# Kernel optimization log

Measured on AMD Instinct MI355X. Metric: run time of the kernel, lower is better.

The kernel has to match this reference:

```python
import jax, jax.numpy as jnp
import numpy as np

EPS = 1e-12  # torch F.normalize default eps


def setup_inputs() -> dict:
    key = jax.random.key(0)
    k1, k2, k3, k4 = jax.random.split(key, 4)
    N, M, V, F, H = 8192, 8192, 3, 512, 512
    common_z = jax.random.normal(k1, (N, F), dtype=jnp.float32)
    zs = jax.random.normal(k2, (V, M, F), dtype=jnp.float32)
    # torch nn.Linear weights have shape [out, in]; kaiming-uniform-ish scale
    s = 1.0 / np.sqrt(F)
    Wq = jax.random.uniform(k3, (H, F), dtype=jnp.float32, minval=-s, maxval=s)
    Wk = jax.random.uniform(k4, (H, F), dtype=jnp.float32, minval=-s, maxval=s)
    return {"common_z": common_z, "zs": zs, "Wq": Wq, "Wk": Wk, "view_num": V}


def reference(common_z, zs, Wq, Wk, view_num):
    # q: [N, H]
    q = jax.nn.elu(common_z @ Wq.T)
    out = common_z
    # view_num is a small fixed structural constant (3); loop over views,
    # matching the original per-view accumulation into common_z.
    for v in range(view_num):
        zv = zs[v]                          # [M, F]
        k = jax.nn.elu(zv @ Wk.T)           # [M, H]
        att = q @ k.T                       # [N, M]
        # row-wise L2 normalize (torch F.normalize p=2, dim=-1)
        norm = jnp.sqrt(jnp.sum(att * att, axis=-1, keepdims=True))
        att = att / jnp.maximum(norm, EPS)
        out = out + att @ zv                # [N, F]
    return out
```

## Files before the change

### kernel.cpp

```cpp
#include <hip/hip_runtime.h>
#include <cstdint>

#define NROWS 8192
#define MDIM  8192
#define FDIM  512
#define HDIM  512
#define GWSPLIT 4

typedef _Float16 f16x8_t __attribute__((ext_vector_type(8)));
typedef float    f32x4_t __attribute__((ext_vector_type(4)));
typedef int      i32x4_t __attribute__((ext_vector_type(4)));

__device__ __forceinline__ unsigned short f2h(float f) {
    return __builtin_bit_cast(unsigned short, (_Float16)f);
}
__device__ __forceinline__ float h2f(unsigned short u) {
    return (float)__builtin_bit_cast(_Float16, u);
}

__device__ __forceinline__ void g2l16(const unsigned short* g, unsigned short* l) {
    __builtin_amdgcn_global_load_lds(
        (const __attribute__((address_space(1))) void*)g,
        (__attribute__((address_space(3))) void*)l, 16, 0, 0);
}

__global__ void k_prep(const float* __restrict__ zs,
                       unsigned short* __restrict__ zn,
                       unsigned short* __restrict__ zt, long tV,
                       const float* __restrict__ cz, unsigned short* __restrict__ cz_h,
                       const float* __restrict__ Wq, unsigned short* __restrict__ wq_h,
                       const float* __restrict__ Wk, unsigned short* __restrict__ wk_h) {
    const long MF = (long)MDIM * FDIM;
    int z = blockIdx.z;
    if (z < 3) {
        const float* src = zs + (long)z * MF;
        unsigned short* dn = zn + (long)z * MF;
        unsigned short* dt = zt + (long)z * tV;
        __shared__ unsigned short t[32][33];
        int c0 = blockIdx.x * 32, r0 = blockIdx.y * 32;
        #pragma unroll
        for (int k = 0; k < 32; k += 8) {
            unsigned short b = f2h(src[(size_t)(r0 + threadIdx.y + k) * FDIM + c0 + threadIdx.x]);
            dn[(size_t)(r0 + threadIdx.y + k) * FDIM + c0 + threadIdx.x] = b;
            t[threadIdx.y + k][threadIdx.x] = b;
        }
        __syncthreads();
        #pragma unroll
        for (int k = 0; k < 32; k += 8)
            dt[(size_t)(c0 + threadIdx.y + k) * MDIM + r0 + threadIdx.x] =
                t[threadIdx.x][threadIdx.y + k];
    } else {
        int tid = threadIdx.y * 32 + threadIdx.x;
        int b = blockIdx.y * gridDim.x + blockIdx.x;
        if (z == 3) {
            int i = b * 256 + tid;
            float4 f = ((const float4*)cz)[i];
            ushort4 u;
            u.x = f2h(f.x); u.y = f2h(f.y); u.z = f2h(f.z); u.w = f2h(f.w);
            ((ushort4*)cz_h)[i] = u;
        } else if (b < 512) {
            const float4* s = (b < 256) ? (const float4*)Wq : (const float4*)Wk;
            ushort4* d = (b < 256) ? (ushort4*)wq_h : (ushort4*)wk_h;
            int i = (b & 255) * 256 + tid;
            float4 f = s[i];
            ushort4 u;
            u.x = f2h(f.x); u.y = f2h(f.y); u.z = f2h(f.z); u.w = f2h(f.w);
            d[i] = u;
        }
    }
}

__global__ void k_rsplit(const float* __restrict__ GWp,
                         unsigned short* __restrict__ G,
                         unsigned short* __restrict__ Bfin,
                         float* __restrict__ n2, int n) {
    int i = blockIdx.x * blockDim.x + threadIdx.x;
    if (i >= n) return;
    if (i < 3 * NROWS) n2[i] = 0.f;
    int v = i / (1024 * 512);
    int rc = i - v * (1024 * 512);
    int row = rc >> 9, col = rc & 511;
    const float* p = GWp + (size_t)v * GWSPLIT * 1024 * 512 + rc;
    float s = 0.f;
    #pragma unroll
    for (int sl = 0; sl < GWSPLIT; ++sl) s += p[(size_t)sl * 1024 * 512];
    if (row < 512) G[((size_t)v * 512 + row) * 512 + col] = f2h(s);
    else Bfin[(size_t)(row - 512) * 1536 + v * 512 + col] = f2h(s);
}

template<int MODE>
__global__ __launch_bounds__(256, 2)
void k_gemm_bt(const unsigned short* __restrict__ A, int lda, long aV, int akmask,
               const unsigned short* __restrict__ B, int ldb, long bV,
               int K, int kslices,
               unsigned short* __restrict__ Cb, long cbV,
               float* __restrict__ Cf, int ldc, long cfV,
               float* __restrict__ norms,
               const unsigned short* __restrict__ Q,
               const float* __restrict__ CZ,
               const unsigned short* __restrict__ B2,
               unsigned short* __restrict__ Cb2) {
    const int z    = blockIdx.z;
    const int view = (MODE == 3) ? z / kslices : z;
    const int kbeg = (MODE == 3) ? (z % kslices) * K : 0;
    A += (long)view * aV;
    const unsigned short* Bp = (MODE == 0 && z > 0) ? B2 : B;
    Bp += (long)view * bV;

    __shared__ unsigned short S[2 * 128 * 64];
    unsigned short* As = S;
    unsigned short* Bs = S + 128 * 64;
    const int tid  = threadIdx.x;
    const int lane = tid & 63;
    const int w    = tid >> 6;
    const int wr   = w >> 1, wc = w & 1;
    const int row0 = blockIdx.y * 128;
    const int col0 = blockIdx.x * 128;
    const int quad = lane >> 4;
    const int l15  = lane & 15;
    const int srow = lane >> 3;
    const int scol = (((lane & 7) ^ srow) * 8);
    const int wbase = w * 4;

    _Float16 sch[3][4];
    if (MODE == 2) {
        #pragma unroll
        for (int v = 0; v < 3; ++v)
            #pragma unroll
            for (int i = 0; i < 4; ++i) {
                int row = row0 + wr * 64 + i * 16 + l15;
                float nn = norms[v * NROWS + row];
                float s = 1.f / fmaxf(sqrtf(fmaxf(nn, 0.f)), 1e-12f);
                sch[v][i] = (_Float16)fminf(s, 60000.f);
            }
    }

    f32x4_t acc[4][4] = {};

    for (int k0 = kbeg; k0 < kbeg + K; k0 += 64) {
        __syncthreads();
        const int ka = k0 & akmask;
        #pragma unroll
        for (int c = 0; c < 4; ++c) {
            int rr = (wbase + c) * 8 + srow;
            g2l16(A  + (size_t)(row0 + rr) * lda + ka + scol, &As[(wbase + c) * 512]);
            g2l16(Bp + (size_t)(col0 + rr) * ldb + k0 + scol, &Bs[(wbase + c) * 512]);
        }
        asm volatile("s_waitcnt vmcnt(0)" ::: "memory");
        __syncthreads();
        #pragma unroll
        for (int kk = 0; kk < 2; ++kk) {
            f16x8_t af[4], bfr[4];
            #pragma unroll
            for (int i = 0; i < 4; ++i) {
                int r = wr * 64 + i * 16 + l15;
                af[i] = __builtin_bit_cast(f16x8_t,
                        *(const i32x4_t*)&As[r * 64 + (((kk * 4 + quad) ^ (r & 7)) << 3)]);
            }
            if (MODE == 2) {
                int vw = k0 >> 9;
                #pragma unroll
                for (int i = 0; i < 4; ++i) af[i] = af[i] * sch[vw][i];
            }
            #pragma unroll
            for (int j = 0; j < 4; ++j) {
                int r = wc * 64 + j * 16 + l15;
                bfr[j] = __builtin_bit_cast(f16x8_t,
                        *(const i32x4_t*)&Bs[r * 64 + (((kk * 4 + quad) ^ (r & 7)) << 3)]);
            }
            #pragma unroll
            for (int i = 0; i < 4; ++i)
                #pragma unroll
                for (int j = 0; j < 4; ++j)
                    acc[i][j] = __builtin_amdgcn_mfma_f32_16x16x32_f16(
                        af[i], bfr[j], acc[i][j], 0, 0, 0);
        }
    }

    if (MODE == 0) {
        if (z == 0) {
            #pragma unroll
            for (int i = 0; i < 4; ++i) {
                int rb = row0 + wr * 64 + i * 16 + quad * 4;
                #pragma unroll
                for (int j = 0; j < 4; ++j) {
                    int col = col0 + wc * 64 + j * 16 + l15;
                    #pragma unroll
                    for (int r = 0; r < 4; ++r) {
                        float v = acc[i][j][r];
                        v = v > 0.f ? v : expm1f(v);
                        Cb[(size_t)(rb + r) * ldc + col] = f2h(v);
                    }
                }
            }
        } else {
            __syncthreads();
            unsigned short* T = S + w * 4096;
            #pragma unroll
            for (int i = 0; i < 4; ++i)
                #pragma unroll
                for (int j = 0; j < 4; ++j) {
                    int ct = j * 16 + l15;
                    #pragma unroll
                    for (int r = 0; r < 4; ++r) {
                        int rt = i * 16 + quad * 4 + r;
                        float v = acc[i][j][r];
                        v = v > 0.f ? v : expm1f(v);
                        T[ct * 64 + (rt ^ ((ct & 7) << 3))] = f2h(v);
                    }
                }
            unsigned short* dst = Cb2 + (long)(z - 1) * cbV;
            #pragma unroll
            for (int it = 0; it < 8; ++it) {
                int c  = it * 8 + (lane >> 3);
                int rg = (lane & 7) * 8;
                i32x4_t val = *(const i32x4_t*)&T[c * 64 + (rg ^ ((c & 7) << 3))];
                *(i32x4_t*)&dst[(size_t)(col0 + wc * 64 + c) * MDIM
                                + row0 + wr * 64 + rg] = val;
            }
        }
    } else if (MODE == 2) {
        #pragma unroll
        for (int i = 0; i < 4; ++i) {
            #pragma unroll
            for (int r = 0; r < 4; ++r) {
                int row = row0 + wr * 64 + i * 16 + quad * 4 + r;
                #pragma unroll
                for (int j = 0; j < 4; ++j) {
                    int col = col0 + wc * 64 + j * 16 + l15;
                    Cf[(size_t)row * ldc + col] =
                        CZ[(size_t)row * ldc + col] + acc[i][j][r];
                }
            }
        }
    } else if (MODE == 3) {
        float* C = Cf + (long)z * cfV;
        #pragma unroll
        for (int i = 0; i < 4; ++i) {
            int rb = row0 + wr * 64 + i * 16 + quad * 4;
            #pragma unroll
            for (int j = 0; j < 4; ++j) {
                int col = col0 + wc * 64 + j * 16 + l15;
                #pragma unroll
                for (int r = 0; r < 4; ++r)
                    C[(size_t)(rb + r) * ldc + col] = acc[i][j][r];
            }
        }
    } else if (MODE == 4) {
        float* nptr = norms + (long)view * NROWS;
        float rs[4][4] = {};
        #pragma unroll
        for (int i = 0; i < 4; ++i) {
            int rb = row0 + wr * 64 + i * 16 + quad * 4;
            #pragma unroll
            for (int j = 0; j < 4; ++j) {
                int col = col0 + wc * 64 + j * 16 + l15;
                #pragma unroll
                for (int r = 0; r < 4; ++r)
                    rs[i][r] += acc[i][j][r] * h2f(Q[(size_t)(rb + r) * ldc + col]);
            }
        }
        #pragma unroll
        for (int i = 0; i < 4; ++i)
            #pragma unroll
            for (int r = 0; r < 4; ++r) {
                float v = rs[i][r];
                v += __shfl_xor(v, 1);
                v += __shfl_xor(v, 2);
                v += __shfl_xor(v, 4);
                v += __shfl_xor(v, 8);
                if (l15 == 0)
                    atomicAdd(&nptr[row0 + wr * 64 + i * 16 + quad * 4 + r], v);
            }
    }
}

extern "C" void kernel_launch(void* const* d_in, const int* in_sizes, int n_in,
                              void* d_out, int out_size, void* d_ws, size_t ws_size,
                              hipStream_t stream) {
    const float* cz = (const float*)d_in[0];
    const float* zs = (const float*)d_in[1];
    const float* Wq = (const float*)d_in[2];
    const float* Wk = (const float*)d_in[3];
    float* out = (float*)d_out;
    const int NOMASK = 0x7fffffff;

    char* ws = (char*)d_ws;
    size_t off = 0;
    auto alloc = [&](size_t bytes) -> void* {
        void* p = ws + off;
        off += (bytes + 255) & ~(size_t)255;
        return p;
    };
    const long MF = (long)MDIM * FDIM;
    const long KZ = (long)1024 * MDIM;

    unsigned short* X_h   = (unsigned short*)alloc((size_t)4 * MF * 2);
    unsigned short* wq_h  = (unsigned short*)alloc((size_t)HDIM * FDIM * 2);
    unsigned short* wk_h  = (unsigned short*)alloc((size_t)HDIM * FDIM * 2);
    unsigned short* q_h   = (unsigned short*)alloc((size_t)NROWS * HDIM * 2);
    unsigned short* kzT   = (unsigned short*)alloc((size_t)3 * KZ * 2);
    float* GWp            = (float*)alloc((size_t)3 * GWSPLIT * 1024 * 512 * 4);
    unsigned short* G     = (unsigned short*)alloc((size_t)3 * 512 * 512 * 2);
    unsigned short* Bfin  = (unsigned short*)alloc((size_t)512 * 1536 * 2);
    float* n2             = (float*)alloc((size_t)3 * NROWS * 4);

    k_prep<<<dim3(FDIM / 32, MDIM / 32, 5), dim3(32, 8), 0, stream>>>(
        zs, X_h + MF, kzT + (size_t)512 * MDIM, KZ,
        cz, X_h, Wq, wq_h, Wk, wk_h);

    k_gemm_bt<0><<<dim3(4, 64, 4), 256, 0, stream>>>(
        X_h, FDIM, MF, NOMASK, wq_h, FDIM, 0, FDIM, 0,
        q_h, KZ, nullptr, HDIM, 0, nullptr, nullptr, nullptr, wk_h, kzT);

    k_gemm_bt<3><<<dim3(4, 8, 3 * GWSPLIT), 256, 0, stream>>>(
        kzT, MDIM, KZ, NOMASK, kzT, MDIM, KZ, MDIM / GWSPLIT, GWSPLIT,
        nullptr, 0, GWp, 512, (long)1024 * 512, nullptr, nullptr, nullptr,
        nullptr, nullptr);

    k_rsplit<<<dim3(3 * 1024 * 512 / 256), 256, 0, stream>>>(
        GWp, G, Bfin, n2, 3 * 1024 * 512);

    k_gemm_bt<4><<<dim3(4, 64, 3), 256, 0, stream>>>(
        q_h, HDIM, 0, NOMASK, G, HDIM, (long)512 * 512, HDIM, 0,
        nullptr, 0, nullptr, HDIM, 0, n2, q_h, nullptr, nullptr, nullptr);

    k_gemm_bt<2><<<dim3(4, 64, 1), 256, 0, stream>>>(
        q_h, HDIM, 0, 511, Bfin, 1536, 0, 1536, 0,
        nullptr, 0, out, FDIM, 0, n2, nullptr, cz, nullptr, nullptr);
}
```

Before: 251.8 us.

## Fuse all stages into one persistent cooperative kernel with grid syncs

Replaces the six separate kernel launches (prep, Wq/Wk projection GEMM, Gram GEMM, split reduction, norm GEMM, final GEMM) with a single cooperative persistent kernel. Each stage becomes a grid-stride job loop, and grid.sync() separates the stages. The aim is to remove launch gaps and inter-kernel idle time. The cost is that the grid size is capped at the occupancy limit, so small stages may underfill the device, and each grid barrier adds its own overhead.

```diff
diff --git a/kernel.cpp b/kernel.cpp
--- a/kernel.cpp
+++ b/kernel.cpp
@@ -1,11 +1,15 @@
 #include <hip/hip_runtime.h>
+#include <hip/hip_cooperative_groups.h>
 #include <cstdint>
+
+namespace cg = cooperative_groups;
 
 #define NROWS 8192
 #define MDIM  8192
 #define FDIM  512
 #define HDIM  512
 #define GWSPLIT 4
+#define NOMASK 0x7fffffff
 
 typedef _Float16 f16x8_t __attribute__((ext_vector_type(8)));
 typedef float    f32x4_t __attribute__((ext_vector_type(4)));
@@ -24,98 +28,42 @@
         (__attribute__((address_space(3))) void*)l, 16, 0, 0);
 }
 
-__global__ void k_prep(const float* __restrict__ zs,
-                       unsigned short* __restrict__ zn,
-                       unsigned short* __restrict__ zt, long tV,
-                       const float* __restrict__ cz, unsigned short* __restrict__ cz_h,
-                       const float* __restrict__ Wq, unsigned short* __restrict__ wq_h,
-                       const float* __restrict__ Wk, unsigned short* __restrict__ wk_h) {
-    const long MF = (long)MDIM * FDIM;
-    int z = blockIdx.z;
-    if (z < 3) {
-        const float* src = zs + (long)z * MF;
-        unsigned short* dn = zn + (long)z * MF;
-        unsigned short* dt = zt + (long)z * tV;
-        __shared__ unsigned short t[32][33];
-        int c0 = blockIdx.x * 32, r0 = blockIdx.y * 32;
-        #pragma unroll
-        for (int k = 0; k < 32; k += 8) {
-            unsigned short b = f2h(src[(size_t)(r0 + threadIdx.y + k) * FDIM + c0 + threadIdx.x]);
-            dn[(size_t)(r0 + threadIdx.y + k) * FDIM + c0 + threadIdx.x] = b;
-            t[threadIdx.y + k][threadIdx.x] = b;
-        }
-        __syncthreads();
-        #pragma unroll
-        for (int k = 0; k < 32; k += 8)
-            dt[(size_t)(c0 + threadIdx.y + k) * MDIM + r0 + threadIdx.x] =
-                t[threadIdx.x][threadIdx.y + k];
-    } else {
-        int tid = threadIdx.y * 32 + threadIdx.x;
-        int b = blockIdx.y * gridDim.x + blockIdx.x;
-        if (z == 3) {
-            int i = b * 256 + tid;
-            float4 f = ((const float4*)cz)[i];
-            ushort4 u;
-            u.x = f2h(f.x); u.y = f2h(f.y); u.z = f2h(f.z); u.w = f2h(f.w);
-            ((ushort4*)cz_h)[i] = u;
-        } else if (b < 512) {
-            const float4* s = (b < 256) ? (const float4*)Wq : (const float4*)Wk;
-            ushort4* d = (b < 256) ? (ushort4*)wq_h : (ushort4*)wk_h;
-            int i = (b & 255) * 256 + tid;
-            float4 f = s[i];
-            ushort4 u;
-            u.x = f2h(f.x); u.y = f2h(f.y); u.z = f2h(f.z); u.w = f2h(f.w);
-            d[i] = u;
-        }
-    }
-}
-
-__global__ void k_rsplit(const float* __restrict__ GWp,
-                         unsigned short* __restrict__ G,
-                         unsigned short* __restrict__ Bfin,
-                         float* __restrict__ n2, int n) {
-    int i = blockIdx.x * blockDim.x + threadIdx.x;
-    if (i >= n) return;
-    if (i < 3 * NROWS) n2[i] = 0.f;
-    int v = i / (1024 * 512);
-    int rc = i - v * (1024 * 512);
-    int row = rc >> 9, col = rc & 511;
-    const float* p = GWp + (size_t)v * GWSPLIT * 1024 * 512 + rc;
-    float s = 0.f;
-    #pragma unroll
-    for (int sl = 0; sl < GWSPLIT; ++sl) s += p[(size_t)sl * 1024 * 512];
-    if (row < 512) G[((size_t)v * 512 + row) * 512 + col] = f2h(s);
-    else Bfin[(size_t)(row - 512) * 1536 + v * 512 + col] = f2h(s);
-}
+struct MegaP {
+    const float* cz; const float* zs; const float* Wq; const float* Wk;
+    float* out;
+    unsigned short* X_h; unsigned short* wq_h; unsigned short* wk_h;
+    unsigned short* q_h; unsigned short* kzT;
+    float* GWp; unsigned short* G; unsigned short* Bfin; float* n2;
+};
 
 template<int MODE>
-__global__ __launch_bounds__(256, 2)
-void k_gemm_bt(const unsigned short* __restrict__ A, int lda, long aV, int akmask,
-               const unsigned short* __restrict__ B, int ldb, long bV,
-               int K, int kslices,
-               unsigned short* __restrict__ Cb, long cbV,
-               float* __restrict__ Cf, int ldc, long cfV,
-               float* __restrict__ norms,
-               const unsigned short* __restrict__ Q,
-               const float* __restrict__ CZ,
-               const unsigned short* __restrict__ B2,
-               unsigned short* __restrict__ Cb2) {
-    const int z    = blockIdx.z;
+__device__ __forceinline__ void gemm_tile(
+    unsigned short* S, int bx, int by, int z,
+    const unsigned short* __restrict__ A, int lda, long aV, int akmask,
+    const unsigned short* __restrict__ B, int ldb, long bV,
+    int K, int kslices,
+    unsigned short* __restrict__ Cb, long cbV, int ldc,
+    float* __restrict__ Cf, long cfV,
+    float* __restrict__ norms,
+    const unsigned short* __restrict__ Q,
+    const float* __restrict__ CZ,
+    const unsigned short* __restrict__ B2,
+    unsigned short* __restrict__ Cb2)
+{
     const int view = (MODE == 3) ? z / kslices : z;
     const int kbeg = (MODE == 3) ? (z % kslices) * K : 0;
     A += (long)view * aV;
     const unsigned short* Bp = (MODE == 0 && z > 0) ? B2 : B;
     Bp += (long)view * bV;
 
-    __shared__ unsigned short S[2 * 128 * 64];
     unsigned short* As = S;
     unsigned short* Bs = S + 128 * 64;
     const int tid  = threadIdx.x;
     const int lane = tid & 63;
     const int w    = tid >> 6;
     const int wr   = w >> 1, wc = w & 1;
-    const int row0 = blockIdx.y * 128;
-    const int col0 = blockIdx.x * 128;
+    const int row0 = by * 128;
+    const int col0 = bx * 128;
     const int quad = lane >> 4;
     const int l15  = lane & 15;
     const int srow = lane >> 3;
@@ -218,6 +166,7 @@
                 *(i32x4_t*)&dst[(size_t)(col0 + wc * 64 + c) * MDIM
                                 + row0 + wr * 64 + rg] = val;
             }
+            __syncthreads();
         }
     } else if (MODE == 2) {
         #pragma unroll
@@ -251,13 +200,14 @@
         float rs[4][4] = {};
         #pragma unroll
         for (int i = 0; i < 4; ++i) {
-            int rb = row0 + wr * 64 + i * 16 + quad * 4;
             #pragma unroll
             for (int j = 0; j < 4; ++j) {
-                int col = col0 + wc * 64 + j * 16 + l15;
-                #pragma unroll
-                for (int r = 0; r < 4; ++r)
+                #pragma unroll
+                for (int r = 0; r < 4; ++r) {
+                    int rb = row0 + wr * 64 + i * 16 + quad * 4;
+                    int col = col0 + wc * 64 + j * 16 + l15;
                     rs[i][r] += acc[i][j][r] * h2f(Q[(size_t)(rb + r) * ldc + col]);
+                }
             }
         }
         #pragma unroll
@@ -275,16 +225,109 @@
     }
 }
 
+__global__ __launch_bounds__(256, 2) void k_mega(MegaP p) {
+    __shared__ unsigned short S[2 * 128 * 64];
+    cg::grid_group grid = cg::this_grid();
+    const int nb  = gridDim.x;
+    const int tid = threadIdx.x;
+    const long MF = (long)MDIM * FDIM;
+    const long KZ = (long)1024 * MDIM;
+
+    for (int job = blockIdx.x; job < 16992; job += nb) {
+        if (job < 12288) {
+            int v = job >> 12, t = job & 4095;
+            int c0 = (t & 15) * 32, r0 = (t >> 4) * 32;
+            int lx = tid & 31, ly = tid >> 5;
+            const float* src = p.zs + (long)v * MF;
+            unsigned short* dn = p.X_h + MF + (long)v * MF;
+            unsigned short* dt = p.kzT + (size_t)512 * MDIM + (long)v * KZ;
+            unsigned short (*t33)[33] = (unsigned short(*)[33])S;
+            #pragma unroll
+            for (int k = 0; k < 32; k += 8) {
+                unsigned short b = f2h(src[(size_t)(r0 + ly + k) * FDIM + c0 + lx]);
+                dn[(size_t)(r0 + ly + k) * FDIM + c0 + lx] = b;
+                t33[ly + k][lx] = b;
+            }
+            __syncthreads();
+            #pragma unroll
+            for (int k = 0; k < 32; k += 8)
+                dt[(size_t)(c0 + ly + k) * MDIM + r0 + lx] = t33[lx][ly + k];
+            __syncthreads();
+        } else if (job < 16384) {
+            int i = (job - 12288) * 256 + tid;
+            float4 f = ((const float4*)p.cz)[i];
+            ushort4 u;
+            u.x = f2h(f.x); u.y = f2h(f.y); u.z = f2h(f.z); u.w = f2h(f.w);
+            ((ushort4*)p.X_h)[i] = u;
+        } else if (job < 16896) {
+            int b = job - 16384;
+            const float4* s = (b < 256) ? (const float4*)p.Wq : (const float4*)p.Wk;
+            ushort4* d = (b < 256) ? (ushort4*)p.wq_h : (ushort4*)p.wk_h;
+            int i = (b & 255) * 256 + tid;
+            float4 f = s[i];
+            ushort4 u;
+            u.x = f2h(f.x); u.y = f2h(f.y); u.z = f2h(f.z); u.w = f2h(f.w);
+            d[i] = u;
+        } else {
+            int idx = (job - 16896) * 256 + tid;
+            if (idx < 3 * NROWS) p.n2[idx] = 0.f;
+        }
+    }
+    grid.sync();
+
+    for (int job = blockIdx.x; job < 1024; job += nb) {
+        int z = job >> 8, r = job & 255;
+        gemm_tile<0>(S, r & 3, r >> 2, z,
+                     p.X_h, FDIM, MF, NOMASK, p.wq_h, FDIM, 0, FDIM, 0,
+                     p.q_h, KZ, HDIM, nullptr, 0,
+                     nullptr, nullptr, nullptr, p.wk_h, p.kzT);
+    }
+    grid.sync();
+
+    for (int job = blockIdx.x; job < 32 * 3 * GWSPLIT; job += nb) {
+        int z = job >> 5, r = job & 31;
+        gemm_tile<3>(S, r & 3, r >> 2, z,
+                     p.kzT, MDIM, KZ, NOMASK, p.kzT, MDIM, KZ,
+                     MDIM / GWSPLIT, GWSPLIT,
+                     nullptr, 0, 512, p.GWp, (long)1024 * 512,
+                     nullptr, nullptr, nullptr, nullptr, nullptr);
+    }
+    grid.sync();
+
+    for (int job = blockIdx.x; job < 6144; job += nb) {
+        int i = job * 256 + tid;
+        int v = i / (1024 * 512);
+        int rc = i - v * (1024 * 512);
+        int row = rc >> 9, col = rc & 511;
+        const float* q = p.GWp + (size_t)v * GWSPLIT * 1024 * 512 + rc;
+        float s = 0.f;
+        #pragma unroll
+        for (int sl = 0; sl < GWSPLIT; ++sl) s += q[(size_t)sl * 1024 * 512];
+        if (row < 512) p.G[((size_t)v * 512 + row) * 512 + col] = f2h(s);
+        else p.Bfin[(size_t)(row - 512) * 1536 + v * 512 + col] = f2h(s);
+    }
+    grid.sync();
+
+    for (int job = blockIdx.x; job < 768; job += nb) {
+        int z = job >> 8, r = job & 255;
+        gemm_tile<4>(S, r & 3, r >> 2, z,
+                     p.q_h, HDIM, 0, NOMASK, p.G, HDIM, (long)512 * 512, HDIM, 0,
+                     nullptr, 0, HDIM, nullptr, 0,
+                     p.n2, p.q_h, nullptr, nullptr, nullptr);
+    }
+    grid.sync();
+
+    for (int job = blockIdx.x; job < 256; job += nb) {
+        gemm_tile<2>(S, job & 3, job >> 2, 0,
+                     p.q_h, HDIM, 0, 511, p.Bfin, 1536, 0, 1536, 0,
+                     nullptr, 0, FDIM, p.out, 0,
+                     p.n2, nullptr, p.cz, nullptr, nullptr);
+    }
+}
+
 extern "C" void kernel_launch(void* const* d_in, const int* in_sizes, int n_in,
                               void* d_out, int out_size, void* d_ws, size_t ws_size,
                               hipStream_t stream) {
-    const float* cz = (const float*)d_in[0];
-    const float* zs = (const float*)d_in[1];
-    const float* Wq = (const float*)d_in[2];
-    const float* Wk = (const float*)d_in[3];
-    float* out = (float*)d_out;
-    const int NOMASK = 0x7fffffff;
-
     char* ws = (char*)d_ws;
     size_t off = 0;
     auto alloc = [&](size_t bytes) -> void* {
@@ -295,37 +338,29 @@
     const long MF = (long)MDIM * FDIM;
     const long KZ = (long)1024 * MDIM;
 
-    unsigned short* X_h   = (unsigned short*)alloc((size_t)4 * MF * 2);
-    unsigned short* wq_h  = (unsigned short*)alloc((size_t)HDIM * FDIM * 2);
-    unsigned short* wk_h  = (unsigned short*)alloc((size_t)HDIM * FDIM * 2);
-    unsigned short* q_h   = (unsigned short*)alloc((size_t)NROWS * HDIM * 2);
-    unsigned short* kzT   = (unsigned short*)alloc((size_t)3 * KZ * 2);
-    float* GWp            = (float*)alloc((size_t)3 * GWSPLIT * 1024 * 512 * 4);
-    unsigned short* G     = (unsigned short*)alloc((size_t)3 * 512 * 512 * 2);
-    unsigned short* Bfin  = (unsigned short*)alloc((size_t)512 * 1536 * 2);
-    float* n2             = (float*)alloc((size_t)3 * NROWS * 4);
-
-    k_prep<<<dim3(FDIM / 32, MDIM / 32, 5), dim3(32, 8), 0, stream>>>(
-        zs, X_h + MF, kzT + (size_t)512 * MDIM, KZ,
-        cz, X_h, Wq, wq_h, Wk, wk_h);
-
-    k_gemm_bt<0><<<dim3(4, 64, 4), 256, 0, stream>>>(
-        X_h, FDIM, MF, NOMASK, wq_h, FDIM, 0, FDIM, 0,
-        q_h, KZ, nullptr, HDIM, 0, nullptr, nullptr, nullptr, wk_h, kzT);
-
-    k_gemm_bt<3><<<dim3(4, 8, 3 * GWSPLIT), 256, 0, stream>>>(
-        kzT, MDIM, KZ, NOMASK, kzT, MDIM, KZ, MDIM / GWSPLIT, GWSPLIT,
-        nullptr, 0, GWp, 512, (long)1024 * 512, nullptr, nullptr, nullptr,
-        nullptr, nullptr);
-
-    k_rsplit<<<dim3(3 * 1024 * 512 / 256), 256, 0, stream>>>(
-        GWp, G, Bfin, n2, 3 * 1024 * 512);
-
-    k_gemm_bt<4><<<dim3(4, 64, 3), 256, 0, stream>>>(
-        q_h, HDIM, 0, NOMASK, G, HDIM, (long)512 * 512, HDIM, 0,
-        nullptr, 0, nullptr, HDIM, 0, n2, q_h, nullptr, nullptr, nullptr);
-
-    k_gemm_bt<2><<<dim3(4, 64, 1), 256, 0, stream>>>(
-        q_h, HDIM, 0, 511, Bfin, 1536, 0, 1536, 0,
-        nullptr, 0, out, FDIM, 0, n2, nullptr, cz, nullptr, nullptr);
-}
+    MegaP p;
+    p.cz = (const float*)d_in[0];
+    p.zs = (const float*)d_in[1];
+    p.Wq = (const float*)d_in[2];
+    p.Wk = (const float*)d_in[3];
+    p.out = (float*)d_out;
+    p.X_h  = (unsigned short*)alloc((size_t)4 * MF * 2);
+    p.wq_h = (unsigned short*)alloc((size_t)HDIM * FDIM * 2);
+    p.wk_h = (unsigned short*)alloc((size_t)HDIM * FDIM * 2);
+    p.q_h  = (unsigned short*)alloc((size_t)NROWS * HDIM * 2);
+    p.kzT  = (unsigned short*)alloc((size_t)3 * KZ * 2);
+    p.GWp  = (float*)alloc((size_t)3 * GWSPLIT * 1024 * 512 * 4);
+    p.G    = (unsigned short*)alloc((size_t)3 * 512 * 512 * 2);
+    p.Bfin = (unsigned short*)alloc((size_t)512 * 1536 * 2);
+    p.n2   = (float*)alloc((size_t)3 * NROWS * 4);
+
+    int ma = 0;
+    hipOccupancyMaxActiveBlocksPerMultiprocessor(&ma, k_mega, 256, 0);
+    if (ma < 1) ma = 1;
+    if (ma > 4) ma = 4;
+    int nblk = ma * 256;
+
+    void* args[] = {&p};
+    hipLaunchCooperativeKernel((void*)k_mega, dim3(nblk), dim3(256),
+                               args, 0, stream);
+}
```

After: 498.6 us. 98.0% more time.

## Double-buffer LDS tiles to overlap global loads with MFMA compute

Applied to the files above, without the earlier changes.

The GEMM main loop gains two LDS buffers, so the next K-tile is prefetched with global_load_lds while MFMAs run on the current one, and only the older loads are waited on (vmcnt(8)). It also raises the GW split-K factor from 4 to 8 to create more blocks. Doubling LDS to 64KB per block may limit how many blocks fit per CU under launch_bounds(256,2), and the raw s_barrier without an LDS wait could be a correctness risk.

```diff
diff --git a/kernel.cpp b/kernel.cpp
--- a/kernel.cpp
+++ b/kernel.cpp
@@ -5,7 +5,8 @@
 #define MDIM  8192
 #define FDIM  512
 #define HDIM  512
-#define GWSPLIT 4
+#define GWSPLIT 8
+#define NOMASK 0x7fffffff
 
 typedef _Float16 f16x8_t __attribute__((ext_vector_type(8)));
 typedef float    f32x4_t __attribute__((ext_vector_type(4)));
@@ -107,9 +108,7 @@
     const unsigned short* Bp = (MODE == 0 && z > 0) ? B2 : B;
     Bp += (long)view * bV;
 
-    __shared__ unsigned short S[2 * 128 * 64];
-    unsigned short* As = S;
-    unsigned short* Bs = S + 128 * 64;
+    __shared__ unsigned short S[4 * 128 * 64];
     const int tid  = threadIdx.x;
     const int lane = tid & 63;
     const int w    = tid >> 6;
@@ -136,18 +135,39 @@
     }
 
     f32x4_t acc[4][4] = {};
-
-    for (int k0 = kbeg; k0 < kbeg + K; k0 += 64) {
-        __syncthreads();
-        const int ka = k0 & akmask;
+    const int nIter = K >> 6;
+
+    {
+        const int ka = kbeg & akmask;
+        unsigned short* As = S;
+        unsigned short* Bs = S + 8192;
         #pragma unroll
         for (int c = 0; c < 4; ++c) {
             int rr = (wbase + c) * 8 + srow;
-            g2l16(A  + (size_t)(row0 + rr) * lda + ka + scol, &As[(wbase + c) * 512]);
-            g2l16(Bp + (size_t)(col0 + rr) * ldb + k0 + scol, &Bs[(wbase + c) * 512]);
-        }
-        asm volatile("s_waitcnt vmcnt(0)" ::: "memory");
-        __syncthreads();
+            g2l16(A  + (size_t)(row0 + rr) * lda + ka   + scol, &As[(wbase + c) * 512]);
+            g2l16(Bp + (size_t)(col0 + rr) * ldb + kbeg + scol, &Bs[(wbase + c) * 512]);
+        }
+    }
+
+    for (int t = 0; t < nIter; ++t) {
+        unsigned short* Asc = S + (t & 1) * 16384;
+        unsigned short* Bsc = Asc + 8192;
+        if (t + 1 < nIter) {
+            const int k1 = kbeg + (t + 1) * 64;
+            const int ka = k1 & akmask;
+            unsigned short* Asn = S + ((t + 1) & 1) * 16384;
+            unsigned short* Bsn = Asn + 8192;
+            #pragma unroll
+            for (int c = 0; c < 4; ++c) {
+                int rr = (wbase + c) * 8 + srow;
+                g2l16(A  + (size_t)(row0 + rr) * lda + ka + scol, &Asn[(wbase + c) * 512]);
+                g2l16(Bp + (size_t)(col0 + rr) * ldb + k1 + scol, &Bsn[(wbase + c) * 512]);
+            }
+            asm volatile("s_waitcnt vmcnt(8)" ::: "memory");
+        } else {
+            asm volatile("s_waitcnt vmcnt(0)" ::: "memory");
+        }
+        __builtin_amdgcn_s_barrier();
         #pragma unroll
         for (int kk = 0; kk < 2; ++kk) {
             f16x8_t af[4], bfr[4];
@@ -155,10 +175,10 @@
             for (int i = 0; i < 4; ++i) {
                 int r = wr * 64 + i * 16 + l15;
                 af[i] = __builtin_bit_cast(f16x8_t,
-                        *(const i32x4_t*)&As[r * 64 + (((kk * 4 + quad) ^ (r & 7)) << 3)]);
+                        *(const i32x4_t*)&Asc[r * 64 + (((kk * 4 + quad) ^ (r & 7)) << 3)]);
             }
             if (MODE == 2) {
-                int vw = k0 >> 9;
+                int vw = (kbeg + t * 64) >> 9;
                 #pragma unroll
                 for (int i = 0; i < 4; ++i) af[i] = af[i] * sch[vw][i];
             }
@@ -166,7 +186,7 @@
             for (int j = 0; j < 4; ++j) {
                 int r = wc * 64 + j * 16 + l15;
                 bfr[j] = __builtin_bit_cast(f16x8_t,
-                        *(const i32x4_t*)&Bs[r * 64 + (((kk * 4 + quad) ^ (r & 7)) << 3)]);
+                        *(const i32x4_t*)&Bsc[r * 64 + (((kk * 4 + quad) ^ (r & 7)) << 3)]);
             }
             #pragma unroll
             for (int i = 0; i < 4; ++i)
@@ -175,6 +195,7 @@
                     acc[i][j] = __builtin_amdgcn_mfma_f32_16x16x32_f16(
                         af[i], bfr[j], acc[i][j], 0, 0, 0);
         }
+        __builtin_amdgcn_s_barrier();
     }
 
     if (MODE == 0) {
@@ -251,13 +272,14 @@
         float rs[4][4] = {};
         #pragma unroll
         for (int i = 0; i < 4; ++i) {
-            int rb = row0 + wr * 64 + i * 16 + quad * 4;
             #pragma unroll
             for (int j = 0; j < 4; ++j) {
-                int col = col0 + wc * 64 + j * 16 + l15;
-                #pragma unroll
-                for (int r = 0; r < 4; ++r)
+                #pragma unroll
+                for (int r = 0; r < 4; ++r) {
+                    int rb = row0 + wr * 64 + i * 16 + quad * 4;
+                    int col = col0 + wc * 64 + j * 16 + l15;
                     rs[i][r] += acc[i][j][r] * h2f(Q[(size_t)(rb + r) * ldc + col]);
+                }
             }
         }
         #pragma unroll
@@ -283,7 +305,6 @@
     const float* Wq = (const float*)d_in[2];
     const float* Wk = (const float*)d_in[3];
     float* out = (float*)d_out;
-    const int NOMASK = 0x7fffffff;
 
     char* ws = (char*)d_ws;
     size_t off = 0;
```

Measured after the change: 261.0 us. 1.04x slower.

## Remap GEMM grids to 1D XCD-aware order, double split-K, store partials in fp16

Applied to the files above, without the earlier changes.

Flattens every GEMM launch to a 1D grid and decodes block indices so that blocks sharing A/B tiles land on the same XCD (block id mod 8), aiming for better L2 reuse on the multi-die GPU. The split-K factor for the kzT Gram GEMM goes from 4 to 8, which gives more blocks for occupancy. Its partial results are now stored as fp16 instead of fp32 to halve partial-sum traffic. The fp16 partials add rounding error before the reduction, and the higher split count means more partials to reduce.

```diff
diff --git a/kernel.cpp b/kernel.cpp
--- a/kernel.cpp
+++ b/kernel.cpp
@@ -5,7 +5,8 @@
 #define MDIM  8192
 #define FDIM  512
 #define HDIM  512
-#define GWSPLIT 4
+#define GWSPLIT 8
+#define NOMASK 0x7fffffff
 
 typedef _Float16 f16x8_t __attribute__((ext_vector_type(8)));
 typedef float    f32x4_t __attribute__((ext_vector_type(4)));
@@ -70,7 +71,7 @@
     }
 }
 
-__global__ void k_rsplit(const float* __restrict__ GWp,
+__global__ void k_rsplit(const unsigned short* __restrict__ GWp,
                          unsigned short* __restrict__ G,
                          unsigned short* __restrict__ Bfin,
                          float* __restrict__ n2, int n) {
@@ -80,10 +81,10 @@
     int v = i / (1024 * 512);
     int rc = i - v * (1024 * 512);
     int row = rc >> 9, col = rc & 511;
-    const float* p = GWp + (size_t)v * GWSPLIT * 1024 * 512 + rc;
+    const unsigned short* p = GWp + (size_t)v * GWSPLIT * 1024 * 512 + rc;
     float s = 0.f;
     #pragma unroll
-    for (int sl = 0; sl < GWSPLIT; ++sl) s += p[(size_t)sl * 1024 * 512];
+    for (int sl = 0; sl < GWSPLIT; ++sl) s += h2f(p[(size_t)sl * 1024 * 512]);
     if (row < 512) G[((size_t)v * 512 + row) * 512 + col] = f2h(s);
     else Bfin[(size_t)(row - 512) * 1536 + v * 512 + col] = f2h(s);
 }
@@ -92,7 +93,7 @@
 __global__ __launch_bounds__(256, 2)
 void k_gemm_bt(const unsigned short* __restrict__ A, int lda, long aV, int akmask,
                const unsigned short* __restrict__ B, int ldb, long bV,
-               int K, int kslices,
+               int K,
                unsigned short* __restrict__ Cb, long cbV,
                float* __restrict__ Cf, int ldc, long cfV,
                float* __restrict__ norms,
@@ -100,12 +101,29 @@
                const float* __restrict__ CZ,
                const unsigned short* __restrict__ B2,
                unsigned short* __restrict__ Cb2) {
-    const int z    = blockIdx.z;
-    const int view = (MODE == 3) ? z / kslices : z;
-    const int kbeg = (MODE == 3) ? (z % kslices) * K : 0;
-    A += (long)view * aV;
+    const int b = blockIdx.x;
+    const int xcd = b & 7, ib = b >> 3;
+    int bx, by, z, kbeg = 0, pidx = 0;
+    if (MODE == 0) {
+        int p = xcd + 8 * (ib >> 2);
+        bx = ib & 3; z = p >> 6; by = p & 63;
+    } else if (MODE == 3) {
+        int s = xcd + 8 * (ib >> 5);
+        int xy = ib & 31;
+        bx = xy & 3; by = xy >> 2;
+        z = s >> 3; kbeg = (s & 7) * K; pidx = s;
+    } else if (MODE == 4) {
+        by = xcd + 8 * (ib / 12);
+        int r = ib % 12;
+        bx = r & 3; z = r >> 2;
+    } else {
+        by = xcd + 8 * (ib >> 2);
+        bx = ib & 3; z = 0;
+    }
+
+    A += (long)z * aV;
     const unsigned short* Bp = (MODE == 0 && z > 0) ? B2 : B;
-    Bp += (long)view * bV;
+    Bp += (long)z * bV;
 
     __shared__ unsigned short S[2 * 128 * 64];
     unsigned short* As = S;
@@ -114,8 +132,8 @@
     const int lane = tid & 63;
     const int w    = tid >> 6;
     const int wr   = w >> 1, wc = w & 1;
-    const int row0 = blockIdx.y * 128;
-    const int col0 = blockIdx.x * 128;
+    const int row0 = by * 128;
+    const int col0 = bx * 128;
     const int quad = lane >> 4;
     const int l15  = lane & 15;
     const int srow = lane >> 3;
@@ -234,7 +252,7 @@
             }
         }
     } else if (MODE == 3) {
-        float* C = Cf + (long)z * cfV;
+        unsigned short* C = Cb + (long)pidx * cbV;
         #pragma unroll
         for (int i = 0; i < 4; ++i) {
             int rb = row0 + wr * 64 + i * 16 + quad * 4;
@@ -243,21 +261,22 @@
                 int col = col0 + wc * 64 + j * 16 + l15;
                 #pragma unroll
                 for (int r = 0; r < 4; ++r)
-                    C[(size_t)(rb + r) * ldc + col] = acc[i][j][r];
+                    C[(size_t)(rb + r) * ldc + col] = f2h(acc[i][j][r]);
             }
         }
     } else if (MODE == 4) {
-        float* nptr = norms + (long)view * NROWS;
+        float* nptr = norms + (long)z * NROWS;
         float rs[4][4] = {};
         #pragma unroll
         for (int i = 0; i < 4; ++i) {
-            int rb = row0 + wr * 64 + i * 16 + quad * 4;
             #pragma unroll
             for (int j = 0; j < 4; ++j) {
-                int col = col0 + wc * 64 + j * 16 + l15;
-                #pragma unroll
-                for (int r = 0; r < 4; ++r)
+                #pragma unroll
+                for (int r = 0; r < 4; ++r) {
+                    int rb = row0 + wr * 64 + i * 16 + quad * 4;
+                    int col = col0 + wc * 64 + j * 16 + l15;
                     rs[i][r] += acc[i][j][r] * h2f(Q[(size_t)(rb + r) * ldc + col]);
+                }
             }
         }
         #pragma unroll
@@ -283,7 +302,6 @@
     const float* Wq = (const float*)d_in[2];
     const float* Wk = (const float*)d_in[3];
     float* out = (float*)d_out;
-    const int NOMASK = 0x7fffffff;
 
     char* ws = (char*)d_ws;
     size_t off = 0;
@@ -294,13 +312,14 @@
     };
     const long MF = (long)MDIM * FDIM;
     const long KZ = (long)1024 * MDIM;
+    const long PS = (long)1024 * 512;
 
     unsigned short* X_h   = (unsigned short*)alloc((size_t)4 * MF * 2);
     unsigned short* wq_h  = (unsigned short*)alloc((size_t)HDIM * FDIM * 2);
     unsigned short* wk_h  = (unsigned short*)alloc((size_t)HDIM * FDIM * 2);
     unsigned short* q_h   = (unsigned short*)alloc((size_t)NROWS * HDIM * 2);
     unsigned short* kzT   = (unsigned short*)alloc((size_t)3 * KZ * 2);
-    float* GWp            = (float*)alloc((size_t)3 * GWSPLIT * 1024 * 512 * 4);
+    unsigned short* GWp   = (unsigned short*)alloc((size_t)3 * GWSPLIT * PS * 2);
     unsigned short* G     = (unsigned short*)alloc((size_t)3 * 512 * 512 * 2);
     unsigned short* Bfin  = (unsigned short*)alloc((size_t)512 * 1536 * 2);
     float* n2             = (float*)alloc((size_t)3 * NROWS * 4);
@@ -309,23 +328,22 @@
         zs, X_h + MF, kzT + (size_t)512 * MDIM, KZ,
         cz, X_h, Wq, wq_h, Wk, wk_h);
 
-    k_gemm_bt<0><<<dim3(4, 64, 4), 256, 0, stream>>>(
-        X_h, FDIM, MF, NOMASK, wq_h, FDIM, 0, FDIM, 0,
+    k_gemm_bt<0><<<dim3(1024), 256, 0, stream>>>(
+        X_h, FDIM, MF, NOMASK, wq_h, FDIM, 0, FDIM,
         q_h, KZ, nullptr, HDIM, 0, nullptr, nullptr, nullptr, wk_h, kzT);
 
-    k_gemm_bt<3><<<dim3(4, 8, 3 * GWSPLIT), 256, 0, stream>>>(
-        kzT, MDIM, KZ, NOMASK, kzT, MDIM, KZ, MDIM / GWSPLIT, GWSPLIT,
-        nullptr, 0, GWp, 512, (long)1024 * 512, nullptr, nullptr, nullptr,
-        nullptr, nullptr);
+    k_gemm_bt<3><<<dim3(768), 256, 0, stream>>>(
+        kzT, MDIM, KZ, NOMASK, kzT, MDIM, KZ, MDIM / GWSPLIT,
+        GWp, PS, nullptr, 512, 0, nullptr, nullptr, nullptr, nullptr, nullptr);
 
     k_rsplit<<<dim3(3 * 1024 * 512 / 256), 256, 0, stream>>>(
         GWp, G, Bfin, n2, 3 * 1024 * 512);
 
-    k_gemm_bt<4><<<dim3(4, 64, 3), 256, 0, stream>>>(
-        q_h, HDIM, 0, NOMASK, G, HDIM, (long)512 * 512, HDIM, 0,
+    k_gemm_bt<4><<<dim3(768), 256, 0, stream>>>(
+        q_h, HDIM, 0, NOMASK, G, HDIM, (long)512 * 512, HDIM,
         nullptr, 0, nullptr, HDIM, 0, n2, q_h, nullptr, nullptr, nullptr);
 
-    k_gemm_bt<2><<<dim3(4, 64, 1), 256, 0, stream>>>(
-        q_h, HDIM, 0, 511, Bfin, 1536, 0, 1536, 0,
+    k_gemm_bt<2><<<dim3(256), 256, 0, stream>>>(
+        q_h, HDIM, 0, 511, Bfin, 1536, 0, 1536,
         nullptr, 0, out, FDIM, 0, n2, nullptr, cz, nullptr, nullptr);
 }
```

After: 240.2 us. 1.05x faster.
